# Kernel optimization log

Hardware: AMD Instinct MI355X
Metric: run time of the kernel (lower is better)

The kernel has to match this reference:

```python
import jax, jax.numpy as jnp
import numpy as np

EPS = 1e-05

def setup_inputs() -> dict:
    key = jax.random.key(0)
    inputs = jax.random.normal(key, (32, 512, 768), dtype=jnp.float32)
    return {"inputs": inputs}

def reference(inputs) -> jnp.ndarray:
    # position weight: L2 norm per token, w[b,l] = sqrt(1e-5 + sum_d x^2)
    w = jnp.sqrt(EPS + jnp.sum(inputs * inputs, axis=-1))  # [B, L]
    # output[b,d,e] = sum_l w[b,l] * x[b,l,d] * x[b,l,e]
    # fused weighted Gram matrix; never materializes [B,L,D,D]
    return jnp.einsum('bld,ble->bde', inputs * w[..., None], inputs)
```

## Files before the change

### kernel.cpp

```cpp
#include <hip/hip_runtime.h>
#include <hip/hip_bf16.h>

#define BATCH 32
#define LL 512
#define DD 768
#define EPSC 1e-5f

typedef __attribute__((ext_vector_type(8))) short bf16x8;
typedef __attribute__((ext_vector_type(4))) float f32x4;

__global__ __launch_bounds__(256) void k_scales(const float* __restrict__ x,
                                                float* __restrict__ s) {
    int wave = threadIdx.x >> 6;
    int lane = threadIdx.x & 63;
    int row = blockIdx.x * 4 + wave;
    const float4* xr = (const float4*)(x + (size_t)row * DD);
    float sum = 0.f;
#pragma unroll
    for (int i = 0; i < 3; i++) {
        float4 v = xr[lane + i * 64];
        sum += v.x * v.x + v.y * v.y + v.z * v.z + v.w * v.w;
    }
#pragma unroll
    for (int off = 32; off > 0; off >>= 1)
        sum += __shfl_xor(sum, off, 64);
    if (lane == 0) s[row] = sqrtf(sqrtf(EPSC + sum));
}

__global__ __launch_bounds__(256) void k_transpose(const float* __restrict__ x,
                                                   const float* __restrict__ s,
                                                   ushort* __restrict__ yt) {
    __shared__ float tile[64][65];
    __shared__ float svec[64];
    int b = blockIdx.z;
    int l0 = blockIdx.y * 64;
    int d0 = blockIdx.x * 64;
    int t = threadIdx.x;
    if (t < 64) svec[t] = s[b * LL + l0 + t];
    const float* xp = x + ((size_t)b * LL + l0) * DD + d0;
    int f = t & 15, lr0 = t >> 4;
#pragma unroll
    for (int r = 0; r < 4; r++) {
        int l = lr0 + r * 16;
        float4 v = *(const float4*)(xp + (size_t)l * DD + f * 4);
#pragma unroll
        for (int j = 0; j < 4; j++)
            tile[l][f * 4 + j] = ((const float*)&v)[j];
    }
    __syncthreads();
    ushort* yp = yt + ((size_t)b * DD + d0) * LL + l0;
    int lc = t & 7, dl0 = t >> 3;
#pragma unroll
    for (int it = 0; it < 2; it++) {
        int d = dl0 + it * 32;
        bf16x8 w;
#pragma unroll
        for (int j = 0; j < 8; j++) {
            int l = lc * 8 + j;
            float v = tile[l][d] * svec[l];
            __hip_bfloat16 h = __float2bfloat16(v);
            w[j] = *(short*)&h;
        }
        *(bf16x8*)(yp + (size_t)d * LL + lc * 8) = w;
    }
}

__global__ __launch_bounds__(256) void k_gemm(const ushort* __restrict__ yt,
                                              float* __restrict__ out) {
    __shared__ ushort At[64 * 32];
    __shared__ ushort Bt[64 * 32];
    int i = blockIdx.x;
    int xcd = i & 7, slot = i >> 3;
    int b = xcd + 8 * (slot / 78);
    int p = slot % 78;
    int t = p, tm = 0, rem = 12;
    while (t >= rem) { t -= rem; rem--; tm++; }
    int tn = tm + t;
    bool diag = (tm == tn);
    int m0 = tm * 64, n0 = tn * 64;
    int tid = threadIdx.x;
    int wave = tid >> 6, lane = tid & 63;
    int wr = wave >> 1, wc = wave & 1;
    const ushort* yb = yt + (size_t)b * DD * LL;

    f32x4 acc[2][2];
#pragma unroll
    for (int ii = 0; ii < 2; ii++)
#pragma unroll
        for (int j = 0; j < 2; j++) acc[ii][j] = (f32x4){0.f, 0.f, 0.f, 0.f};

    int srow = lane >> 2;
    int ssw = (srow ^ (srow >> 1)) & 3;
    int scol = ((lane & 3) ^ ssw) * 8;
    int fr = lane & 15;
    int fsw = (fr ^ (fr >> 1)) & 3;
    int fslot = (lane >> 4) ^ fsw;

    for (int ks = 0; ks < 16; ks++) {
        int k0 = ks * 32;
        __syncthreads();
        {
            int rloc = wave * 16 + srow;
            const ushort* gA = yb + (size_t)(m0 + rloc) * LL + k0 + scol;
            __builtin_amdgcn_global_load_lds(
                (const __attribute__((address_space(1))) void*)gA,
                (__attribute__((address_space(3))) void*)(At + (wave * 16) * 32),
                16, 0, 0);
            if (!diag) {
                const ushort* gB = yb + (size_t)(n0 + rloc) * LL + k0 + scol;
                __builtin_amdgcn_global_load_lds(
                    (const __attribute__((address_space(1))) void*)gB,
                    (__attribute__((address_space(3))) void*)(Bt + (wave * 16) * 32),
                    16, 0, 0);
            }
        }
        __syncthreads();

        const ushort* Bsrc = diag ? At : Bt;
        bf16x8 afrag[2], bfrag[2];
#pragma unroll
        for (int ii = 0; ii < 2; ii++) {
            int m = wr * 32 + ii * 16 + fr;
            afrag[ii] = *(const bf16x8*)(At + m * 32 + fslot * 8);
            int n = wc * 32 + ii * 16 + fr;
            bfrag[ii] = *(const bf16x8*)(Bsrc + n * 32 + fslot * 8);
        }
#pragma unroll
        for (int ii = 0; ii < 2; ii++)
#pragma unroll
            for (int j = 0; j < 2; j++)
                acc[ii][j] = __builtin_amdgcn_mfma_f32_16x16x32_bf16(
                    afrag[ii], bfrag[j], acc[ii][j], 0, 0, 0);
    }

    float* op = out + (size_t)b * DD * DD;
#pragma unroll
    for (int ii = 0; ii < 2; ii++) {
        int colb = m0 + wr * 32 + ii * 16 + (lane >> 4) * 4;
#pragma unroll
        for (int j = 0; j < 2; j++) {
            int row = n0 + wc * 32 + j * 16 + fr;
            float4 v = {acc[ii][j][0], acc[ii][j][1], acc[ii][j][2], acc[ii][j][3]};
            *(float4*)(op + (size_t)row * DD + colb) = v;
        }
    }
    if (!diag) {
#pragma unroll
        for (int ii = 0; ii < 2; ii++) {
            int mbase = m0 + wr * 32 + ii * 16 + (lane >> 4) * 4;
#pragma unroll
            for (int j = 0; j < 2; j++) {
                int n = n0 + wc * 32 + j * 16 + fr;
#pragma unroll
                for (int r = 0; r < 4; r++)
                    op[(size_t)(mbase + r) * DD + n] = acc[ii][j][r];
            }
        }
    }
}

extern "C" void kernel_launch(void* const* d_in, const int* in_sizes, int n_in,
                              void* d_out, int out_size, void* d_ws, size_t ws_size,
                              hipStream_t stream) {
    const float* x = (const float*)d_in[0];
    float* s = (float*)d_ws;
    ushort* yt = (ushort*)((char*)d_ws + 65536);

    k_scales<<<dim3((BATCH * LL) / 4), 256, 0, stream>>>(x, s);
    k_transpose<<<dim3(DD / 64, LL / 64, BATCH), 256, 0, stream>>>(x, s, yt);
    k_gemm<<<dim3(78 * BATCH), 256, 0, stream>>>(yt, (float*)d_out);
}
```

Measured before the change: 135.5 us.

## Compute each 64x64 Gram tile with one wave loading fragments from global

The GEMM block shrinks from four waves to a single 64-lane wave that computes the full 64x64 output tile with a 4x4 array of MFMA accumulators. Operand fragments are loaded straight from global memory into registers, so the LDS staging and both per-step barriers are gone. This removes sync overhead and LDS traffic and reuses each fragment across four MFMAs instead of two. In exchange it uses more registers per thread, leaves fewer waves per block to hide latency, and relies on cache hits for the uncoalesced 16-byte row loads.

New measurement: 159.0 us. 1.17x slower.

```diff
diff --git a/kernel.cpp b/kernel.cpp
--- a/kernel.cpp
+++ b/kernel.cpp
@@ -65,10 +65,8 @@
     }
 }
 
-__global__ __launch_bounds__(256) void k_gemm(const ushort* __restrict__ yt,
-                                              float* __restrict__ out) {
-    __shared__ ushort At[64 * 32];
-    __shared__ ushort Bt[64 * 32];
+__global__ __launch_bounds__(64) void k_gemm(const ushort* __restrict__ yt,
+                                             float* __restrict__ out) {
     int i = blockIdx.x;
     int xcd = i & 7, slot = i >> 3;
     int b = xcd + 8 * (slot / 78);
@@ -78,79 +76,54 @@
     int tn = tm + t;
     bool diag = (tm == tn);
     int m0 = tm * 64, n0 = tn * 64;
-    int tid = threadIdx.x;
-    int wave = tid >> 6, lane = tid & 63;
-    int wr = wave >> 1, wc = wave & 1;
+    int lane = threadIdx.x;
+    int fr = lane & 15, ks4 = lane >> 4;
     const ushort* yb = yt + (size_t)b * DD * LL;
+    const ushort* pa = yb + (size_t)(m0 + fr) * LL + ks4 * 8;
+    const ushort* pb = yb + (size_t)(n0 + fr) * LL + ks4 * 8;
+    if (diag) pb = pa;
 
-    f32x4 acc[2][2];
+    f32x4 acc[4][4];
 #pragma unroll
-    for (int ii = 0; ii < 2; ii++)
+    for (int ii = 0; ii < 4; ii++)
 #pragma unroll
-        for (int j = 0; j < 2; j++) acc[ii][j] = (f32x4){0.f, 0.f, 0.f, 0.f};
+        for (int j = 0; j < 4; j++) acc[ii][j] = (f32x4){0.f, 0.f, 0.f, 0.f};
 
-    int srow = lane >> 2;
-    int ssw = (srow ^ (srow >> 1)) & 3;
-    int scol = ((lane & 3) ^ ssw) * 8;
-    int fr = lane & 15;
-    int fsw = (fr ^ (fr >> 1)) & 3;
-    int fslot = (lane >> 4) ^ fsw;
-
+#pragma unroll 2
     for (int ks = 0; ks < 16; ks++) {
-        int k0 = ks * 32;
-        __syncthreads();
-        {
-            int rloc = wave * 16 + srow;
-            const ushort* gA = yb + (size_t)(m0 + rloc) * LL + k0 + scol;
-            __builtin_amdgcn_global_load_lds(
-                (const __attribute__((address_space(1))) void*)gA,
-                (__attribute__((address_space(3))) void*)(At + (wave * 16) * 32),
-                16, 0, 0);
-            if (!diag) {
-                const ushort* gB = yb + (size_t)(n0 + rloc) * LL + k0 + scol;
-                __builtin_amdgcn_global_load_lds(
-                    (const __attribute__((address_space(1))) void*)gB,
-                    (__attribute__((address_space(3))) void*)(Bt + (wave * 16) * 32),
-                    16, 0, 0);
-            }
-        }
-        __syncthreads();
-
-        const ushort* Bsrc = diag ? At : Bt;
-        bf16x8 afrag[2], bfrag[2];
+        bf16x8 af[4], bg[4];
 #pragma unroll
-        for (int ii = 0; ii < 2; ii++) {
-            int m = wr * 32 + ii * 16 + fr;
-            afrag[ii] = *(const bf16x8*)(At + m * 32 + fslot * 8);
-            int n = wc * 32 + ii * 16 + fr;
-            bfrag[ii] = *(const bf16x8*)(Bsrc + n * 32 + fslot * 8);
-        }
+        for (int ii = 0; ii < 4; ii++)
+            af[ii] = *(const bf16x8*)(pa + (size_t)ii * 16 * LL + ks * 32);
 #pragma unroll
-        for (int ii = 0; ii < 2; ii++)
+        for (int j = 0; j < 4; j++)
+            bg[j] = *(const bf16x8*)(pb + (size_t)j * 16 * LL + ks * 32);
 #pragma unroll
-            for (int j = 0; j < 2; j++)
+        for (int ii = 0; ii < 4; ii++)
+#pragma unroll
+            for (int j = 0; j < 4; j++)
                 acc[ii][j] = __builtin_amdgcn_mfma_f32_16x16x32_bf16(
-                    afrag[ii], bfrag[j], acc[ii][j], 0, 0, 0);
+                    af[ii], bg[j], acc[ii][j], 0, 0, 0);
     }
 
     float* op = out + (size_t)b * DD * DD;
 #pragma unroll
-    for (int ii = 0; ii < 2; ii++) {
-        int colb = m0 + wr * 32 + ii * 16 + (lane >> 4) * 4;
+    for (int ii = 0; ii < 4; ii++) {
+        int colb = m0 + ii * 16 + ks4 * 4;
 #pragma unroll
-        for (int j = 0; j < 2; j++) {
-            int row = n0 + wc * 32 + j * 16 + fr;
+        for (int j = 0; j < 4; j++) {
+            int row = n0 + j * 16 + fr;
             float4 v = {acc[ii][j][0], acc[ii][j][1], acc[ii][j][2], acc[ii][j][3]};
             *(float4*)(op + (size_t)row * DD + colb) = v;
         }
     }
     if (!diag) {
 #pragma unroll
-        for (int ii = 0; ii < 2; ii++) {
-            int mbase = m0 + wr * 32 + ii * 16 + (lane >> 4) * 4;
+        for (int ii = 0; ii < 4; ii++) {
+            int mbase = m0 + ii * 16 + ks4 * 4;
 #pragma unroll
-            for (int j = 0; j < 2; j++) {
-                int n = n0 + wc * 32 + j * 16 + fr;
+            for (int j = 0; j < 4; j++) {
+                int n = n0 + j * 16 + fr;
 #pragma unroll
                 for (int r = 0; r < 4; r++)
                     op[(size_t)(mbase + r) * DD + n] = acc[ii][j][r];
@@ -168,5 +141,5 @@
 
     k_scales<<<dim3((BATCH * LL) / 4), 256, 0, stream>>>(x, s);
     k_transpose<<<dim3(DD / 64, LL / 64, BATCH), 256, 0, stream>>>(x, s, yt);
-    k_gemm<<<dim3(78 * BATCH), 256, 0, stream>>>(yt, (float*)d_out);
+    k_gemm<<<dim3(78 * BATCH), 64, 0, stream>>>(yt, (float*)d_out);
 }
```
